# Kernel tuning notes

Measured on AMD Instinct MI355X. Metric: run time of the kernel, lower is better.

## Reference

```python
import jax, jax.numpy as jnp
import numpy as np

B, S, HID = 2, 1024, 2048
HQ, HKV, HD = 32, 8, 64
ROPE_BASE = 10000.0

def _rope_tables(seq_len, head_dim):
    inv_freq = 1.0 / (ROPE_BASE ** (np.arange(0, head_dim, 2, dtype=np.float32) / head_dim))
    t = np.arange(seq_len, dtype=np.float32)
    freqs = np.outer(t, inv_freq)                      # [S, d/2]
    emb = np.concatenate([freqs, freqs], axis=-1)      # [S, d]
    return jnp.asarray(np.cos(emb)), jnp.asarray(np.sin(emb))

def setup_inputs() -> dict:
    key = jax.random.key(0)
    ks = jax.random.split(key, 5)
    cos, sin = _rope_tables(S, HD)
    return {
        'hidden_states': jax.random.normal(ks[0], (B, S, HID), jnp.float32),
        'cos': cos, 'sin': sin,
        'Wq': jax.random.normal(ks[1], (HID, HID), jnp.float32) * (HID ** -0.5),
        'Wk': jax.random.normal(ks[2], (HID, HKV * HD), jnp.float32) * (HID ** -0.5),
        'Wv': jax.random.normal(ks[3], (HID, HKV * HD), jnp.float32) * (HID ** -0.5),
        'Wo': jax.random.normal(ks[4], (HID, HID), jnp.float32) * (HID ** -0.5),
    }

def _rotate_half(x):
    d = x.shape[-1]
    return jnp.concatenate([-x[..., d // 2:], x[..., :d // 2]], axis=-1)

def reference(hidden_states, cos, sin, Wq, Wk, Wv, Wo):
    b, s, _ = hidden_states.shape
    q = (hidden_states @ Wq).reshape(b, s, HQ, HD)    # [b,s,Hq,d]
    k = (hidden_states @ Wk).reshape(b, s, HKV, HD)   # [b,s,Hkv,d]
    v = (hidden_states @ Wv).reshape(b, s, HKV, HD)
    # RoPE: cos/sin [s,d] broadcast as [s,1,d] over head dim
    c = cos[:, None, :]
    sn = sin[:, None, :]
    q = q * c + _rotate_half(q) * sn
    k = k * c + _rotate_half(k) * sn
    # GQA: expand kv heads to query heads (repeat_kv)
    n_rep = HQ // HKV
    k = jnp.repeat(k, n_rep, axis=2)                  # [b,s,Hq,d]
    v = jnp.repeat(v, n_rep, axis=2)
    scale = HD ** -0.5
    scores = jnp.einsum('bqhd,bkhd->bhqk', q, k) * scale  # [b,Hq,s,s]
    causal = jnp.tril(jnp.ones((s, s), bool))
    scores = jnp.where(causal, scores, jnp.float32(-1e30))
    probs = jax.nn.softmax(scores.astype(jnp.float32), axis=-1).astype(q.dtype)
    out = jnp.einsum('bhqk,bkhd->bqhd', probs, v).reshape(b, s, HID)
    return out @ Wo
```

## Files before the change

kernel.cpp:

```cpp
#include <hip/hip_runtime.h>
#include <math.h>

#define B_   2
#define S_   1024
#define HID_ 2048
#define HQ_  32
#define HKV_ 8
#define HD_  64
#define NQKV 3072

using short8  = __attribute__((ext_vector_type(8))) short;
using floatx4 = __attribute__((ext_vector_type(4))) float;

__device__ __forceinline__ unsigned short f2bf(float x) {
    unsigned int u = __builtin_bit_cast(unsigned int, x);
    u += 0x7FFFu + ((u >> 16) & 1u);
    return (unsigned short)(u >> 16);
}
__device__ __forceinline__ float bf2f(unsigned short u) {
    return __builtin_bit_cast(float, (unsigned int)u << 16);
}

__device__ __forceinline__ void gl_lds16(const unsigned short* g, unsigned short* l) {
    __builtin_amdgcn_global_load_lds(
        (const __attribute__((address_space(1))) void*)g,
        (__attribute__((address_space(3))) void*)l, 16, 0, 0);
}

template <bool BF16OUT>
__global__ __launch_bounds__(256) void gemm_mfma(const unsigned short* __restrict__ A,
                                                 const unsigned short* __restrict__ Bt,
                                                 void* __restrict__ Cv,
                                                 int M, int N, int K) {
    __shared__ __align__(16) unsigned short As[128 * 32];
    __shared__ __align__(16) unsigned short Bs[128 * 32];

    const int tid  = threadIdx.x;
    const int w    = tid >> 6;
    const int lane = tid & 63;
    const int col  = lane & 15;
    const int quad = lane >> 4;
    const int m0 = blockIdx.y * 128;
    const int n0 = blockIdx.x * 128;
    const int wm = (w >> 1) * 64;
    const int wn = (w & 1) * 64;

    const int srow = lane >> 2;
    const int skof = (lane & 3) * 8;
    const unsigned short* Ag = A  + (size_t)(m0 + srow) * K + skof;
    const unsigned short* Bg = Bt + (size_t)(n0 + srow) * K + skof;
    const int rb = w * 16;

    floatx4 acc[4][4] = {};

    for (int k0 = 0; k0 < K; k0 += 32) {
        gl_lds16(Ag + (size_t)(rb     ) * K + k0, &As[(rb     ) * 32]);
        gl_lds16(Ag + (size_t)(rb + 64) * K + k0, &As[(rb + 64) * 32]);
        gl_lds16(Bg + (size_t)(rb     ) * K + k0, &Bs[(rb     ) * 32]);
        gl_lds16(Bg + (size_t)(rb + 64) * K + k0, &Bs[(rb + 64) * 32]);
        __syncthreads();

        short8 af[4], bfr[4];
#pragma unroll
        for (int i = 0; i < 4; ++i)
            af[i] = *(const short8*)&As[(wm + i * 16 + col) * 32 + quad * 8];
#pragma unroll
        for (int j = 0; j < 4; ++j)
            bfr[j] = *(const short8*)&Bs[(wn + j * 16 + col) * 32 + quad * 8];
#pragma unroll
        for (int i = 0; i < 4; ++i)
#pragma unroll
            for (int j = 0; j < 4; ++j)
                acc[i][j] = __builtin_amdgcn_mfma_f32_16x16x32_bf16(
                    af[i], bfr[j], acc[i][j], 0, 0, 0);
        __syncthreads();
    }

#pragma unroll
    for (int i = 0; i < 4; ++i)
#pragma unroll
        for (int j = 0; j < 4; ++j)
#pragma unroll
            for (int r = 0; r < 4; ++r) {
                size_t off = (size_t)(m0 + wm + i * 16 + quad * 4 + r) * N
                           + (n0 + wn + j * 16 + col);
                if constexpr (BF16OUT)
                    ((unsigned short*)Cv)[off] = f2bf(acc[i][j][r]);
                else
                    ((float*)Cv)[off] = acc[i][j][r];
            }
}

__global__ __launch_bounds__(256) void convert_x(const float* __restrict__ in,
                                                 unsigned short* __restrict__ out) {
    int tid = blockIdx.x * 256 + threadIdx.x;
    float4 v = *(const float4*)&in[(size_t)tid * 4];
    ushort4 o = {f2bf(v.x), f2bf(v.y), f2bf(v.z), f2bf(v.w)};
    *(ushort4*)&out[(size_t)tid * 4] = o;
}

__global__ __launch_bounds__(256) void transpose_all(const float* __restrict__ Wq,
                                                     const float* __restrict__ Wk,
                                                     const float* __restrict__ Wv,
                                                     const float* __restrict__ Wo,
                                                     unsigned short* __restrict__ WcatT,
                                                     unsigned short* __restrict__ WoT) {
    __shared__ float tile[32][33];
    int bid = blockIdx.x;
    const float* W;
    unsigned short* WT;
    int N, tn0, tk0;
    if (bid < 4096) {
        W = Wq; WT = WcatT; N = HID_;
        tn0 = (bid & 63) * 32; tk0 = (bid >> 6) * 32;
    } else if (bid < 5120) {
        bid -= 4096;
        W = Wk; WT = WcatT + (size_t)HID_ * HID_; N = 512;
        tn0 = (bid & 15) * 32; tk0 = (bid >> 4) * 32;
    } else if (bid < 6144) {
        bid -= 5120;
        W = Wv; WT = WcatT + (size_t)(HID_ + 512) * HID_; N = 512;
        tn0 = (bid & 15) * 32; tk0 = (bid >> 4) * 32;
    } else {
        bid -= 6144;
        W = Wo; WT = WoT; N = HID_;
        tn0 = (bid & 63) * 32; tk0 = (bid >> 6) * 32;
    }
    const int r  = threadIdx.x >> 3;
    const int c4 = (threadIdx.x & 7) * 4;
    float4 v = *(const float4*)&W[(size_t)(tk0 + r) * N + tn0 + c4];
    tile[r][c4 + 0] = v.x;
    tile[r][c4 + 1] = v.y;
    tile[r][c4 + 2] = v.z;
    tile[r][c4 + 3] = v.w;
    __syncthreads();
    ushort4 o = {f2bf(tile[c4 + 0][r]), f2bf(tile[c4 + 1][r]),
                 f2bf(tile[c4 + 2][r]), f2bf(tile[c4 + 3][r])};
    *(ushort4*)&WT[(size_t)(tn0 + r) * HID_ + tk0 + c4] = o;
}

__global__ __launch_bounds__(256) void convert_qkv(const unsigned short* __restrict__ QKV,
                                                   const float* __restrict__ cosT,
                                                   const float* __restrict__ sinT,
                                                   unsigned short* __restrict__ Qbf,
                                                   unsigned short* __restrict__ Kbf,
                                                   unsigned short* __restrict__ Vt) {
    int tid = blockIdx.x * 256 + threadIdx.x;
    const int NQ = B_ * S_ * HQ_ * 32;
    const int NK = B_ * S_ * HKV_ * 32;
    if (tid < NQ) {
        int d = tid & 31;
        int h = (tid >> 5) & (HQ_ - 1);
        int s = (tid >> 10) & (S_ - 1);
        int b = tid >> 20;
        const unsigned short* row = QKV + (size_t)(b * S_ + s) * NQKV + h * HD_;
        float x0 = bf2f(row[d]), x1 = bf2f(row[d + 32]);
        float c0 = cosT[s * HD_ + d],      s0 = sinT[s * HD_ + d];
        float c1 = cosT[s * HD_ + d + 32], s1 = sinT[s * HD_ + d + 32];
        unsigned short* orow = Qbf + ((size_t)(b * HQ_ + h) * S_ + s) * HD_;
        orow[d]      = f2bf((x0 * c0 - x1 * s0) * 0.125f);
        orow[d + 32] = f2bf((x1 * c1 + x0 * s1) * 0.125f);
    } else if (tid < NQ + NK) {
        tid -= NQ;
        int d  = tid & 31;
        int kv = (tid >> 5) & (HKV_ - 1);
        int s  = (tid >> 8) & (S_ - 1);
        int b  = tid >> 18;
        const unsigned short* row = QKV + (size_t)(b * S_ + s) * NQKV + HID_ + kv * HD_;
        float x0 = bf2f(row[d]), x1 = bf2f(row[d + 32]);
        float c0 = cosT[s * HD_ + d],      s0 = sinT[s * HD_ + d];
        float c1 = cosT[s * HD_ + d + 32], s1 = sinT[s * HD_ + d + 32];
        unsigned short* orow = Kbf + ((size_t)(b * HKV_ + kv) * S_ + s) * HD_;
        orow[d]      = f2bf(x0 * c0 - x1 * s0);
        orow[d + 32] = f2bf(x1 * c1 + x0 * s1);
    } else {
        tid -= NQ + NK;
        int s4 = tid & 255;
        int d  = (tid >> 8) & (HD_ - 1);
        int kv = (tid >> 14) & (HKV_ - 1);
        int b  = tid >> 17;
        int s  = s4 * 4;
        const unsigned short* base =
            QKV + (size_t)b * S_ * NQKV + HID_ + 512 + kv * HD_ + d;
        ushort4 o;
        o.x = base[(size_t)(s + 0) * NQKV];
        o.y = base[(size_t)(s + 1) * NQKV];
        o.z = base[(size_t)(s + 2) * NQKV];
        o.w = base[(size_t)(s + 3) * NQKV];
        *(ushort4*)&Vt[((size_t)(b * HKV_ + kv) * HD_ + d) * S_ + s] = o;
    }
}

__global__ __launch_bounds__(256) void attn_mfma(const unsigned short* __restrict__ Qbf,
                                                 const unsigned short* __restrict__ Kbf,
                                                 const unsigned short* __restrict__ Vt,
                                                 unsigned short* __restrict__ Ctx) {
    const int t  = 63 - blockIdx.x;
    const int kv = blockIdx.y;
    const int b  = blockIdx.z;
    const int w    = threadIdx.x >> 6;
    const int lane = threadIdx.x & 63;
    const int col  = lane & 15;
    const int quad = lane >> 4;

    const int h   = kv * 4 + w;
    const int bh  = b * HQ_ + h;
    const int bkv = b * HKV_ + kv;
    const int qw  = 16 * t;
    const int myq = qw + col;

    __shared__ __align__(16) unsigned short sK[2][64 * 32];
    __shared__ __align__(16) unsigned short sV[2][64 * 32];
    __shared__ __align__(16) unsigned short sP[4][16 * 72];
    unsigned short* myP = sP[w];

    const unsigned short* qrow = Qbf + ((size_t)bh * S_ + qw + col) * HD_;
    short8 bq0 = *(const short8*)&qrow[quad * 8];
    short8 bq1 = *(const short8*)&qrow[32 + quad * 8];

    const unsigned short* Kbase = Kbf + (size_t)bkv * S_ * HD_;
    const unsigned short* Vbase = Vt  + (size_t)bkv * HD_ * S_;

    const int srow = 16 * w + (lane >> 2);
    const int sch  = (lane & 3) * 8;
    unsigned short* dK0 = &sK[0][16 * w * 32];
    unsigned short* dK1 = &sK[1][16 * w * 32];
    unsigned short* dV0 = &sV[0][16 * w * 32];
    unsigned short* dV1 = &sV[1][16 * w * 32];

    floatx4 acc[4] = {};
    float m_i = -1e30f, l_i = 0.f;
    const int nsteps = (16 * t + 79) >> 6;

    for (int it = 0; it < nsteps; ++it) {
        const int k0 = it * 64;
        gl_lds16(Kbase + (size_t)(k0 + srow) * HD_ + sch,      dK0);
        gl_lds16(Kbase + (size_t)(k0 + srow) * HD_ + 32 + sch, dK1);
        gl_lds16(Vbase + (size_t)srow * S_ + k0 + sch,         dV0);
        gl_lds16(Vbase + (size_t)srow * S_ + k0 + 32 + sch,    dV1);
        __syncthreads();

        floatx4 sc[4];
#pragma unroll
        for (int tt = 0; tt < 4; ++tt) {
            short8 ak0 = *(const short8*)&sK[0][(16 * tt + col) * 32 + quad * 8];
            short8 ak1 = *(const short8*)&sK[1][(16 * tt + col) * 32 + quad * 8];
            floatx4 z = {0.f, 0.f, 0.f, 0.f};
            z = __builtin_amdgcn_mfma_f32_16x16x32_bf16(ak0, bq0, z, 0, 0, 0);
            z = __builtin_amdgcn_mfma_f32_16x16x32_bf16(ak1, bq1, z, 0, 0, 0);
            sc[tt] = z;
        }
        if (k0 + 63 > qw) {
#pragma unroll
            for (int tt = 0; tt < 4; ++tt)
#pragma unroll
                for (int r = 0; r < 4; ++r)
                    if (k0 + 16 * tt + quad * 4 + r > myq) sc[tt][r] = -1e30f;
        }
        float vmax = sc[0][0];
#pragma unroll
        for (int tt = 0; tt < 4; ++tt)
#pragma unroll
            for (int r = 0; r < 4; ++r)
                vmax = fmaxf(vmax, sc[tt][r]);
        vmax = fmaxf(vmax, __shfl_xor(vmax, 16, 64));
        vmax = fmaxf(vmax, __shfl_xor(vmax, 32, 64));
        const float mnew  = fmaxf(m_i, vmax);
        const float alpha = __expf(m_i - mnew);
        m_i = mnew;
        float lsum = 0.f;
#pragma unroll
        for (int tt = 0; tt < 4; ++tt) {
            float p0 = __expf(sc[tt][0] - mnew);
            float p1 = __expf(sc[tt][1] - mnew);
            float p2 = __expf(sc[tt][2] - mnew);
            float p3 = __expf(sc[tt][3] - mnew);
            lsum += (p0 + p1) + (p2 + p3);
            ushort4 pk = {f2bf(p0), f2bf(p1), f2bf(p2), f2bf(p3)};
            *(ushort4*)&myP[col * 72 + 16 * tt + quad * 4] = pk;
        }
        lsum += __shfl_xor(lsum, 16, 64);
        lsum += __shfl_xor(lsum, 32, 64);
        l_i = l_i * alpha + lsum;
        float a_r[4];
#pragma unroll
        for (int r = 0; r < 4; ++r)
            a_r[r] = __shfl(alpha, quad * 4 + r, 64);
#pragma unroll
        for (int nt = 0; nt < 4; ++nt)
#pragma unroll
            for (int r = 0; r < 4; ++r)
                acc[nt][r] *= a_r[r];
        short8 pa0 = *(const short8*)&myP[col * 72 + quad * 8];
        short8 pa1 = *(const short8*)&myP[col * 72 + 32 + quad * 8];
#pragma unroll
        for (int nt = 0; nt < 4; ++nt) {
            short8 vb0 = *(const short8*)&sV[0][(nt * 16 + col) * 32 + quad * 8];
            short8 vb1 = *(const short8*)&sV[1][(nt * 16 + col) * 32 + quad * 8];
            acc[nt] = __builtin_amdgcn_mfma_f32_16x16x32_bf16(pa0, vb0, acc[nt], 0, 0, 0);
            acc[nt] = __builtin_amdgcn_mfma_f32_16x16x32_bf16(pa1, vb1, acc[nt], 0, 0, 0);
        }
        __syncthreads();
    }

    const float invl = 1.0f / l_i;
    float inv_r[4];
#pragma unroll
    for (int r = 0; r < 4; ++r)
        inv_r[r] = __shfl(invl, quad * 4 + r, 64);
#pragma unroll
    for (int nt = 0; nt < 4; ++nt)
#pragma unroll
        for (int r = 0; r < 4; ++r)
            Ctx[(size_t)(b * S_ + qw + quad * 4 + r) * HID_ + h * HD_ + nt * 16 + col] =
                f2bf(acc[nt][r] * inv_r[r]);
}

extern "C" void kernel_launch(void* const* d_in, const int* in_sizes, int n_in,
                              void* d_out, int out_size, void* d_ws, size_t ws_size,
                              hipStream_t stream) {
    const float* X    = (const float*)d_in[0];
    const float* cosT = (const float*)d_in[1];
    const float* sinT = (const float*)d_in[2];
    const float* Wq   = (const float*)d_in[3];
    const float* Wk   = (const float*)d_in[4];
    const float* Wv   = (const float*)d_in[5];
    const float* Wo   = (const float*)d_in[6];

    const int M = B_ * S_;
    const size_t MB = 1024u * 1024u;

    char* ws = (char*)d_ws;
    unsigned short* Xbf   = (unsigned short*)(ws);
    unsigned short* Qbf   = (unsigned short*)(ws);
    unsigned short* WcatT = (unsigned short*)(ws + 8 * MB);
    unsigned short* Kbf   = (unsigned short*)(ws + 8 * MB);
    unsigned short* Vt    = (unsigned short*)(ws + 10 * MB);
    unsigned short* Ctxbf = (unsigned short*)(ws + 12 * MB);
    unsigned short* WoT   = (unsigned short*)(ws + 20 * MB);
    unsigned short* QKVbf = (unsigned short*)d_out;
    float* out = (float*)d_out;

    convert_x<<<(M * HID_ / 4) / 256, 256, 0, stream>>>(X, Xbf);

    transpose_all<<<10240, 256, 0, stream>>>(Wq, Wk, Wv, Wo, WcatT, WoT);

    gemm_mfma<true><<<dim3(NQKV / 128, M / 128), 256, 0, stream>>>(
        Xbf, WcatT, QKVbf, M, NQKV, HID_);

    {
        int total = B_ * S_ * HQ_ * 32 + B_ * S_ * HKV_ * 32
                  + B_ * HKV_ * HD_ * (S_ / 4);
        convert_qkv<<<total / 256, 256, 0, stream>>>(QKVbf, cosT, sinT, Qbf, Kbf, Vt);
    }

    attn_mfma<<<dim3(64, HKV_, B_), 256, 0, stream>>>(Qbf, Kbf, Vt, Ctxbf);

    gemm_mfma<false><<<dim3(HID_ / 128, M / 128), 256, 0, stream>>>(
        Ctxbf, WoT, out, M, HID_, HID_);
}
```

Baseline: 263.0 us.

## Split-K both GEMMs into two halves with bf16 partials and fused reduction

Both projection GEMMs are split along K into two halves, doubling the block count (QKV: 384 to 768 blocks, Wo: 256 to 512) so the 256-CU device stays better occupied. The QKV partials are summed inside the RoPE/convert kernel. The Wo partials are combined by a new reduce kernel that adds the bf16 second half into the fp32 output. The Wo transpose is also split out and launched later. In exchange this writes and reads extra partial buffers, adds a kernel launch, and rounds the partials to bf16, which costs some precision.

```diff
diff --git a/kernel.cpp b/kernel.cpp
--- a/kernel.cpp
+++ b/kernel.cpp
@@ -27,37 +27,47 @@
         (__attribute__((address_space(3))) void*)l, 16, 0, 0);
 }
 
-template <bool BF16OUT>
-__global__ __launch_bounds__(256) void gemm_mfma(const unsigned short* __restrict__ A,
-                                                 const unsigned short* __restrict__ Bt,
-                                                 void* __restrict__ Cv,
-                                                 int M, int N, int K) {
+__global__ __launch_bounds__(256) void gemm_qkv(const unsigned short* __restrict__ A,
+                                                const unsigned short* __restrict__ Bt,
+                                                unsigned short* __restrict__ Qp,
+                                                unsigned short* __restrict__ KVp) {
     __shared__ __align__(16) unsigned short As[128 * 32];
     __shared__ __align__(16) unsigned short Bs[128 * 32];
+
+    int bid = blockIdx.x;
+    int m0, n0, z, Nw, nc0;
+    unsigned short* C;
+    if (bid < 512) {
+        n0 = (bid & 15) * 128; m0 = ((bid >> 4) & 15) * 128; z = bid >> 8;
+        C = Qp + (size_t)z * 2048 * 2048; Nw = 2048; nc0 = n0;
+    } else {
+        bid -= 512;
+        n0 = 2048 + (bid & 7) * 128; m0 = ((bid >> 3) & 15) * 128; z = bid >> 7;
+        C = KVp + (size_t)z * 2048 * 1024; Nw = 1024; nc0 = n0 - 2048;
+    }
+    const int kbase = z * 1024;
 
     const int tid  = threadIdx.x;
     const int w    = tid >> 6;
     const int lane = tid & 63;
     const int col  = lane & 15;
     const int quad = lane >> 4;
-    const int m0 = blockIdx.y * 128;
-    const int n0 = blockIdx.x * 128;
     const int wm = (w >> 1) * 64;
     const int wn = (w & 1) * 64;
 
     const int srow = lane >> 2;
     const int skof = (lane & 3) * 8;
-    const unsigned short* Ag = A  + (size_t)(m0 + srow) * K + skof;
-    const unsigned short* Bg = Bt + (size_t)(n0 + srow) * K + skof;
+    const unsigned short* Ag = A  + (size_t)(m0 + srow) * HID_ + skof;
+    const unsigned short* Bg = Bt + (size_t)(n0 + srow) * HID_ + skof;
     const int rb = w * 16;
 
     floatx4 acc[4][4] = {};
 
-    for (int k0 = 0; k0 < K; k0 += 32) {
-        gl_lds16(Ag + (size_t)(rb     ) * K + k0, &As[(rb     ) * 32]);
-        gl_lds16(Ag + (size_t)(rb + 64) * K + k0, &As[(rb + 64) * 32]);
-        gl_lds16(Bg + (size_t)(rb     ) * K + k0, &Bs[(rb     ) * 32]);
-        gl_lds16(Bg + (size_t)(rb + 64) * K + k0, &Bs[(rb + 64) * 32]);
+    for (int k0 = kbase; k0 < kbase + 1024; k0 += 32) {
+        gl_lds16(Ag + (size_t)(rb     ) * HID_ + k0, &As[(rb     ) * 32]);
+        gl_lds16(Ag + (size_t)(rb + 64) * HID_ + k0, &As[(rb + 64) * 32]);
+        gl_lds16(Bg + (size_t)(rb     ) * HID_ + k0, &Bs[(rb     ) * 32]);
+        gl_lds16(Bg + (size_t)(rb + 64) * HID_ + k0, &Bs[(rb + 64) * 32]);
         __syncthreads();
 
         short8 af[4], bfr[4];
@@ -81,14 +91,82 @@
 #pragma unroll
         for (int j = 0; j < 4; ++j)
 #pragma unroll
+            for (int r = 0; r < 4; ++r)
+                C[(size_t)(m0 + wm + i * 16 + quad * 4 + r) * Nw
+                  + (nc0 + wn + j * 16 + col)] = f2bf(acc[i][j][r]);
+}
+
+__global__ __launch_bounds__(256) void gemm_wo(const unsigned short* __restrict__ A,
+                                               const unsigned short* __restrict__ Bt,
+                                               float* __restrict__ Cf,
+                                               unsigned short* __restrict__ Cp1) {
+    __shared__ __align__(16) unsigned short As[128 * 32];
+    __shared__ __align__(16) unsigned short Bs[128 * 32];
+
+    const int m0 = blockIdx.y * 128;
+    const int n0 = blockIdx.x * 128;
+    const int z  = blockIdx.z;
+    const int kbase = z * 1024;
+
+    const int tid  = threadIdx.x;
+    const int w    = tid >> 6;
+    const int lane = tid & 63;
+    const int col  = lane & 15;
+    const int quad = lane >> 4;
+    const int wm = (w >> 1) * 64;
+    const int wn = (w & 1) * 64;
+
+    const int srow = lane >> 2;
+    const int skof = (lane & 3) * 8;
+    const unsigned short* Ag = A  + (size_t)(m0 + srow) * HID_ + skof;
+    const unsigned short* Bg = Bt + (size_t)(n0 + srow) * HID_ + skof;
+    const int rb = w * 16;
+
+    floatx4 acc[4][4] = {};
+
+    for (int k0 = kbase; k0 < kbase + 1024; k0 += 32) {
+        gl_lds16(Ag + (size_t)(rb     ) * HID_ + k0, &As[(rb     ) * 32]);
+        gl_lds16(Ag + (size_t)(rb + 64) * HID_ + k0, &As[(rb + 64) * 32]);
+        gl_lds16(Bg + (size_t)(rb     ) * HID_ + k0, &Bs[(rb     ) * 32]);
+        gl_lds16(Bg + (size_t)(rb + 64) * HID_ + k0, &Bs[(rb + 64) * 32]);
+        __syncthreads();
+
+        short8 af[4], bfr[4];
+#pragma unroll
+        for (int i = 0; i < 4; ++i)
+            af[i] = *(const short8*)&As[(wm + i * 16 + col) * 32 + quad * 8];
+#pragma unroll
+        for (int j = 0; j < 4; ++j)
+            bfr[j] = *(const short8*)&Bs[(wn + j * 16 + col) * 32 + quad * 8];
+#pragma unroll
+        for (int i = 0; i < 4; ++i)
+#pragma unroll
+            for (int j = 0; j < 4; ++j)
+                acc[i][j] = __builtin_amdgcn_mfma_f32_16x16x32_bf16(
+                    af[i], bfr[j], acc[i][j], 0, 0, 0);
+        __syncthreads();
+    }
+
+#pragma unroll
+    for (int i = 0; i < 4; ++i)
+#pragma unroll
+        for (int j = 0; j < 4; ++j)
+#pragma unroll
             for (int r = 0; r < 4; ++r) {
-                size_t off = (size_t)(m0 + wm + i * 16 + quad * 4 + r) * N
+                size_t off = (size_t)(m0 + wm + i * 16 + quad * 4 + r) * HID_
                            + (n0 + wn + j * 16 + col);
-                if constexpr (BF16OUT)
-                    ((unsigned short*)Cv)[off] = f2bf(acc[i][j][r]);
-                else
-                    ((float*)Cv)[off] = acc[i][j][r];
+                if (z == 0) Cf[off] = acc[i][j][r];
+                else        Cp1[off] = f2bf(acc[i][j][r]);
             }
+}
+
+__global__ __launch_bounds__(256) void reduce_wo(float* __restrict__ out,
+                                                 const unsigned short* __restrict__ p1) {
+    int i4 = (blockIdx.x * 256 + threadIdx.x) * 4;
+    float4 o = *(float4*)&out[i4];
+    ushort4 p = *(const ushort4*)&p1[i4];
+    o.x += bf2f(p.x); o.y += bf2f(p.y); o.z += bf2f(p.z); o.w += bf2f(p.w);
+    *(float4*)&out[i4] = o;
 }
 
 __global__ __launch_bounds__(256) void convert_x(const float* __restrict__ in,
@@ -99,12 +177,10 @@
     *(ushort4*)&out[(size_t)tid * 4] = o;
 }
 
-__global__ __launch_bounds__(256) void transpose_all(const float* __restrict__ Wq,
+__global__ __launch_bounds__(256) void transpose_qkv(const float* __restrict__ Wq,
                                                      const float* __restrict__ Wk,
                                                      const float* __restrict__ Wv,
-                                                     const float* __restrict__ Wo,
-                                                     unsigned short* __restrict__ WcatT,
-                                                     unsigned short* __restrict__ WoT) {
+                                                     unsigned short* __restrict__ WcatT) {
     __shared__ float tile[32][33];
     int bid = blockIdx.x;
     const float* W;
@@ -117,14 +193,10 @@
         bid -= 4096;
         W = Wk; WT = WcatT + (size_t)HID_ * HID_; N = 512;
         tn0 = (bid & 15) * 32; tk0 = (bid >> 4) * 32;
-    } else if (bid < 6144) {
+    } else {
         bid -= 5120;
         W = Wv; WT = WcatT + (size_t)(HID_ + 512) * HID_; N = 512;
         tn0 = (bid & 15) * 32; tk0 = (bid >> 4) * 32;
-    } else {
-        bid -= 6144;
-        W = Wo; WT = WoT; N = HID_;
-        tn0 = (bid & 63) * 32; tk0 = (bid >> 6) * 32;
     }
     const int r  = threadIdx.x >> 3;
     const int c4 = (threadIdx.x & 7) * 4;
@@ -139,12 +211,34 @@
     *(ushort4*)&WT[(size_t)(tn0 + r) * HID_ + tk0 + c4] = o;
 }
 
-__global__ __launch_bounds__(256) void convert_qkv(const unsigned short* __restrict__ QKV,
+__global__ __launch_bounds__(256) void transpose_wo(const float* __restrict__ Wo,
+                                                    unsigned short* __restrict__ WoT) {
+    __shared__ float tile[32][33];
+    int bid = blockIdx.x;
+    const int tn0 = (bid & 63) * 32;
+    const int tk0 = (bid >> 6) * 32;
+    const int r  = threadIdx.x >> 3;
+    const int c4 = (threadIdx.x & 7) * 4;
+    float4 v = *(const float4*)&Wo[(size_t)(tk0 + r) * HID_ + tn0 + c4];
+    tile[r][c4 + 0] = v.x;
+    tile[r][c4 + 1] = v.y;
+    tile[r][c4 + 2] = v.z;
+    tile[r][c4 + 3] = v.w;
+    __syncthreads();
+    ushort4 o = {f2bf(tile[c4 + 0][r]), f2bf(tile[c4 + 1][r]),
+                 f2bf(tile[c4 + 2][r]), f2bf(tile[c4 + 3][r])};
+    *(ushort4*)&WoT[(size_t)(tn0 + r) * HID_ + tk0 + c4] = o;
+}
+
+__global__ __launch_bounds__(256) void convert_qkv(const unsigned short* __restrict__ Qp,
+                                                   const unsigned short* __restrict__ KVp,
                                                    const float* __restrict__ cosT,
                                                    const float* __restrict__ sinT,
                                                    unsigned short* __restrict__ Qbf,
                                                    unsigned short* __restrict__ Kbf,
                                                    unsigned short* __restrict__ Vt) {
+    const size_t QSTR  = (size_t)2048 * 2048;
+    const size_t KVSTR = (size_t)2048 * 1024;
     int tid = blockIdx.x * 256 + threadIdx.x;
     const int NQ = B_ * S_ * HQ_ * 32;
     const int NK = B_ * S_ * HKV_ * 32;
@@ -153,8 +247,9 @@
         int h = (tid >> 5) & (HQ_ - 1);
         int s = (tid >> 10) & (S_ - 1);
         int b = tid >> 20;
-        const unsigned short* row = QKV + (size_t)(b * S_ + s) * NQKV + h * HD_;
-        float x0 = bf2f(row[d]), x1 = bf2f(row[d + 32]);
+        const unsigned short* row = Qp + (size_t)(b * S_ + s) * 2048 + h * HD_;
+        float x0 = bf2f(row[d])      + bf2f(row[QSTR + d]);
+        float x1 = bf2f(row[d + 32]) + bf2f(row[QSTR + d + 32]);
         float c0 = cosT[s * HD_ + d],      s0 = sinT[s * HD_ + d];
         float c1 = cosT[s * HD_ + d + 32], s1 = sinT[s * HD_ + d + 32];
         unsigned short* orow = Qbf + ((size_t)(b * HQ_ + h) * S_ + s) * HD_;
@@ -166,8 +261,9 @@
         int kv = (tid >> 5) & (HKV_ - 1);
         int s  = (tid >> 8) & (S_ - 1);
         int b  = tid >> 18;
-        const unsigned short* row = QKV + (size_t)(b * S_ + s) * NQKV + HID_ + kv * HD_;
-        float x0 = bf2f(row[d]), x1 = bf2f(row[d + 32]);
+        const unsigned short* row = KVp + (size_t)(b * S_ + s) * 1024 + kv * HD_;
+        float x0 = bf2f(row[d])      + bf2f(row[KVSTR + d]);
+        float x1 = bf2f(row[d + 32]) + bf2f(row[KVSTR + d + 32]);
         float c0 = cosT[s * HD_ + d],      s0 = sinT[s * HD_ + d];
         float c1 = cosT[s * HD_ + d + 32], s1 = sinT[s * HD_ + d + 32];
         unsigned short* orow = Kbf + ((size_t)(b * HKV_ + kv) * S_ + s) * HD_;
@@ -181,12 +277,14 @@
         int b  = tid >> 17;
         int s  = s4 * 4;
         const unsigned short* base =
-            QKV + (size_t)b * S_ * NQKV + HID_ + 512 + kv * HD_ + d;
+            KVp + ((size_t)(b * S_ + s)) * 1024 + 512 + kv * HD_ + d;
         ushort4 o;
-        o.x = base[(size_t)(s + 0) * NQKV];
-        o.y = base[(size_t)(s + 1) * NQKV];
-        o.z = base[(size_t)(s + 2) * NQKV];
-        o.w = base[(size_t)(s + 3) * NQKV];
+#pragma unroll
+        for (int j = 0; j < 4; ++j) {
+            float v = bf2f(base[(size_t)j * 1024]) +
+                      bf2f(base[KVSTR + (size_t)j * 1024]);
+            ((unsigned short*)&o)[j] = f2bf(v);
+        }
         *(ushort4*)&Vt[((size_t)(b * HKV_ + kv) * HD_ + d) * S_ + s] = o;
     }
 }
@@ -336,26 +434,31 @@
     unsigned short* WcatT = (unsigned short*)(ws + 8 * MB);
     unsigned short* Kbf   = (unsigned short*)(ws + 8 * MB);
     unsigned short* Vt    = (unsigned short*)(ws + 10 * MB);
-    unsigned short* Ctxbf = (unsigned short*)(ws + 12 * MB);
-    unsigned short* WoT   = (unsigned short*)(ws + 20 * MB);
-    unsigned short* QKVbf = (unsigned short*)d_out;
+    unsigned short* WoT   = (unsigned short*)(ws + 12 * MB);
+    unsigned short* KVp   = (unsigned short*)(ws + 20 * MB);
+    unsigned short* Ctxbf = (unsigned short*)(ws + 20 * MB);
+    unsigned short* Wop1  = (unsigned short*)(ws);
+    unsigned short* Qp    = (unsigned short*)d_out;
     float* out = (float*)d_out;
 
     convert_x<<<(M * HID_ / 4) / 256, 256, 0, stream>>>(X, Xbf);
 
-    transpose_all<<<10240, 256, 0, stream>>>(Wq, Wk, Wv, Wo, WcatT, WoT);
-
-    gemm_mfma<true><<<dim3(NQKV / 128, M / 128), 256, 0, stream>>>(
-        Xbf, WcatT, QKVbf, M, NQKV, HID_);
+    transpose_qkv<<<6144, 256, 0, stream>>>(Wq, Wk, Wv, WcatT);
+
+    gemm_qkv<<<768, 256, 0, stream>>>(Xbf, WcatT, Qp, KVp);
 
     {
         int total = B_ * S_ * HQ_ * 32 + B_ * S_ * HKV_ * 32
                   + B_ * HKV_ * HD_ * (S_ / 4);
-        convert_qkv<<<total / 256, 256, 0, stream>>>(QKVbf, cosT, sinT, Qbf, Kbf, Vt);
-    }
+        convert_qkv<<<total / 256, 256, 0, stream>>>(Qp, KVp, cosT, sinT,
+                                                     Qbf, Kbf, Vt);
+    }
+
+    transpose_wo<<<4096, 256, 0, stream>>>(Wo, WoT);
 
     attn_mfma<<<dim3(64, HKV_, B_), 256, 0, stream>>>(Qbf, Kbf, Vt, Ctxbf);
 
-    gemm_mfma<false><<<dim3(HID_ / 128, M / 128), 256, 0, stream>>>(
-        Ctxbf, WoT, out, M, HID_, HID_);
-}
+    gemm_wo<<<dim3(16, 16, 2), 256, 0, stream>>>(Ctxbf, WoT, out, Wop1);
+
+    reduce_wo<<<(M * HID_ / 4) / 256, 256, 0, stream>>>(out, Wop1);
+}
```

Result: faster. 245.6 us (-6.6%).
